# Kernel optimization log

Hardware: AMD Instinct MI355X
Metric: run time of the kernel (lower is better)

## Reference

```python
import jax, jax.numpy as jnp
import numpy as np

B, N, M, V = 256, 16, 128, 64
H, K = 256, 8
TYPES, SPANS = 12, 15          # types 9..20, spans 2..16
TAU = 1.0
NEG = -1e30


def setup_inputs() -> dict:
    key = jax.random.key(0)
    ks = jax.random.split(key, 8)
    decodings = jax.random.normal(ks[0], (B, N, M, V), jnp.float32)
    variables = jax.random.normal(ks[1], (B, N, 30, 3, V), jnp.float32)
    target_types = 9 + jax.random.randint(ks[2], (B,), 0, TYPES)      # [9, 20]
    spans = 2 + jax.random.randint(ks[3], (B,), 0, SPANS)             # [2, 16]
    type_emb_table = jax.random.normal(ks[4], (21, H), jnp.float32)
    W_sem = jax.random.normal(ks[5], (SPANS, TYPES, H, K * (N + 1)), jnp.float32) * 0.05
    b_sem = jnp.zeros((SPANS, TYPES, K * (N + 1)), jnp.float32)
    u = jax.random.uniform(ks[6], (B, K, N + 1), jnp.float32, 1e-9, 1.0)
    gumbel = -jnp.log(-jnp.log(u))
    return dict(decodings=decodings, variables=variables, target_types=target_types,
                spans=spans, type_emb_table=type_emb_table, W_sem=W_sem,
                b_sem=b_sem, gumbel=gumbel)


def _dt_sample(type_emb_table, W_sem, b_sem, gumbel, target_types, spans):
    te = type_emb_table[target_types]                                  # [B,H]
    Wg = W_sem[spans - 2, target_types - 9]                            # [B,H,K*(N+1)]
    bg = b_sem[spans - 2, target_types - 9]                            # [B,K*(N+1)]
    logits = (jnp.einsum('bh,bho->bo', te, Wg) + bg).reshape(B, K, N + 1)
    valid = jnp.arange(N + 1)[None, None, :] < (spans[:, None, None] + 1)
    logits = jnp.where(valid, logits, NEG)
    logp = jax.nn.log_softmax(logits, axis=-1)
    y_soft = jax.nn.softmax((logp + gumbel) / TAU, axis=-1)
    hard = jax.nn.one_hot(jnp.argmax(y_soft, axis=-1), N + 1, dtype=y_soft.dtype)
    dt = hard + y_soft - jax.lax.stop_gradient(y_soft)                 # straight-through
    dt = jnp.where(valid, dt, 0.0)                                     # zeros beyond span+1
    # type 20 uses the fixed start template: template 0 picks decoding 0, rest pick pad
    start = jax.nn.one_hot(jnp.where(jnp.arange(K) == 0, 1, 0), N + 1, dtype=dt.dtype)
    return jnp.where((target_types == 20)[:, None, None], start[None], dt)


def _apply_decoder_template(dt, decodings):
    pad = jnp.zeros((M, V), decodings.dtype).at[:, 0].set(1.0)         # pad token one-hot
    choices = jnp.concatenate(
        [jnp.broadcast_to(pad.reshape(1, 1, M * V), (B, 1, M * V)),
         decodings.reshape(B, N, M * V)], axis=1)                      # [B,N+1,M*V]
    outputs = jnp.einsum('bkn,bnf->bkf', dt, choices).reshape(B, K, M, V)

    jpos = jnp.arange(M, dtype=jnp.int32)

    def step(carry, out_t):                                            # out_t: [B,M,V]
        result, idx = carry
        out_idx = jnp.argmax(out_t, axis=-1)                           # [B,M]
        olen = jnp.max(jnp.where(out_idx != 0, jpos + 1, 0), axis=-1)  # last non-pad + 1
        olen = jnp.minimum(olen, M - idx)
        rel = jpos[None, :] - idx[:, None]                             # [B,M]
        take = (rel >= 0) & (rel < olen[:, None])
        gathered = jnp.take_along_axis(out_t, jnp.clip(rel, 0, M - 1)[:, :, None], axis=1)
        result = jnp.where(take[:, :, None], gathered, result)
        return (result, idx + olen), None

    init = (jnp.zeros((B, M, V), decodings.dtype), jnp.zeros((B,), jnp.int32))
    (result, _), _ = jax.lax.scan(step, init, jnp.moveaxis(outputs, 1, 0))
    return result


def reference(decodings, variables, target_types, spans, type_emb_table, W_sem, b_sem, gumbel):
    dt = _dt_sample(type_emb_table, W_sem, b_sem, gumbel, target_types, spans)
    new_d = _apply_decoder_template(dt, decodings)
    new_v = jnp.zeros((B, 40, 3, V), decodings.dtype)
    return new_d, new_v
```

## Files before the change

kernel.cpp:

```cpp
#include <hip/hip_runtime.h>
#include <cfloat>

constexpr int B_ = 256, N_ = 16, M_ = 128, V_ = 64, H_ = 256, K_ = 8, NP1 = 17;
constexpr int KO = K_ * NP1;
constexpr int TYPES_ = 12;

__global__ __launch_bounds__(256) void fused_template_kernel(
    const float* __restrict__ decodings,
    const int*   __restrict__ target_types,
    const int*   __restrict__ spans,
    const float* __restrict__ type_emb,
    const float* __restrict__ W_sem,
    const float* __restrict__ b_sem,
    const float* __restrict__ gumbel,
    float* __restrict__ out_d,
    float* __restrict__ out_v)
{
    const int b = blockIdx.x;
    const int t = threadIdx.x;

    __shared__ float te[H_];
    __shared__ float score[KO];
    __shared__ int   sel[K_];
    __shared__ int   wave_hi[2];

    const int tt = target_types[b];
    const int sp = spans[b];

    if (tt == 20) {
        if (t < K_) sel[t] = (t == 0) ? 1 : 0;
    } else {
        te[t] = type_emb[tt * H_ + t];
        __syncthreads();
        const int row = (sp - 2) * TYPES_ + (tt - 9);
        if (t < KO) {
            const float* W = W_sem + (size_t)row * H_ * KO + t;
            float acc = b_sem[row * KO + t];
            #pragma unroll 8
            for (int h = 0; h < H_; ++h)
                acc = fmaf(te[h], W[(size_t)h * KO], acc);
            const int n = t % NP1;
            const float g = gumbel[b * KO + t];
            score[t] = (n <= sp) ? (acc + g) : -FLT_MAX;
        }
        __syncthreads();
        if (t < K_) {
            float bv = score[t * NP1];
            int bi = 0;
            for (int n = 1; n < NP1; ++n) {
                float v = score[t * NP1 + n];
                if (v > bv) { bv = v; bi = n; }
            }
            sel[t] = bi;
        }
    }
    __syncthreads();

    int idx = 0;
    for (int k = 0; k < K_; ++k) {
        if (idx >= M_) break;
        const int s = sel[k];
        if (s == 0) continue;
        const float* seq = decodings + ((size_t)b * N_ + (s - 1)) * (M_ * V_);

        int nonpad = 0;
        if (t < M_) {
            const float4* p = reinterpret_cast<const float4*>(seq + t * V_);
            float bv = -FLT_MAX; int bi = 0;
            #pragma unroll
            for (int q = 0; q < V_ / 4; ++q) {
                float4 x = p[q];
                if (x.x > bv) { bv = x.x; bi = 4 * q + 0; }
                if (x.y > bv) { bv = x.y; bi = 4 * q + 1; }
                if (x.z > bv) { bv = x.z; bi = 4 * q + 2; }
                if (x.w > bv) { bv = x.w; bi = 4 * q + 3; }
            }
            nonpad = (bi != 0);
        }
        const unsigned long long mask = __ballot(nonpad);
        if ((t & 63) == 0 && (t >> 6) < 2)
            wave_hi[t >> 6] = mask ? (63 - __clzll(mask)) : -1;
        __syncthreads();
        int olen = (wave_hi[1] >= 0) ? (wave_hi[1] + 65) : (wave_hi[0] + 1);
        olen = min(olen, M_ - idx);

        const int cnt4 = olen * (V_ / 4);
        const float4* src4 = reinterpret_cast<const float4*>(seq);
        float4* dst4 = reinterpret_cast<float4*>(out_d + ((size_t)b * M_ + idx) * V_);
        for (int i = t; i < cnt4; i += 256) dst4[i] = src4[i];
        idx += olen;
        __syncthreads();
    }

    const float4 z = make_float4(0.f, 0.f, 0.f, 0.f);
    float4* db = reinterpret_cast<float4*>(out_d + (size_t)b * M_ * V_);
    for (int i = idx * (V_ / 4) + t; i < M_ * (V_ / 4); i += 256) db[i] = z;
    float4* dv = reinterpret_cast<float4*>(out_v + (size_t)b * (40 * 3 * V_));
    for (int i = t; i < (40 * 3 * V_) / 4; i += 256) dv[i] = z;
}

extern "C" void kernel_launch(void* const* d_in, const int* in_sizes, int n_in,
                              void* d_out, int out_size, void* d_ws, size_t ws_size,
                              hipStream_t stream) {
    const float* decodings    = (const float*)d_in[0];
    const int*   target_types = (const int*)d_in[2];
    const int*   spans        = (const int*)d_in[3];
    const float* type_emb     = (const float*)d_in[4];
    const float* W_sem        = (const float*)d_in[5];
    const float* b_sem        = (const float*)d_in[6];
    const float* gumbel       = (const float*)d_in[7];

    float* out_d = (float*)d_out;
    float* out_v = out_d + (size_t)B_ * M_ * V_;

    fused_template_kernel<<<dim3(B_), dim3(256), 0, stream>>>(
        decodings, target_types, spans, type_emb, W_sem, b_sem, gumbel, out_d, out_v);
}
```

Before: 247.2 us.

## Stage W_sem rows through LDS with all threads and split zeroing into extra blocks

After: 251.0 us. About the same (+1.5%).

```diff
diff --git a/kernel.cpp b/kernel.cpp
--- a/kernel.cpp
+++ b/kernel.cpp
@@ -4,6 +4,8 @@
 constexpr int B_ = 256, N_ = 16, M_ = 128, V_ = 64, H_ = 256, K_ = 8, NP1 = 17;
 constexpr int KO = K_ * NP1;
 constexpr int TYPES_ = 12;
+constexpr int CHUNK = 64;
+constexpr int NV_F4 = (40 * 3 * V_) / 4;
 
 __global__ __launch_bounds__(256) void fused_template_kernel(
     const float* __restrict__ decodings,
@@ -16,9 +18,20 @@
     float* __restrict__ out_d,
     float* __restrict__ out_v)
 {
+    const int t = threadIdx.x;
+    const float4 z = make_float4(0.f, 0.f, 0.f, 0.f);
+
+    if (blockIdx.x >= B_) {
+        const int zb = blockIdx.x - B_;
+        float4* dv = reinterpret_cast<float4*>(out_v + (size_t)zb * (NV_F4 * 4));
+        #pragma unroll
+        for (int i = t; i < NV_F4; i += 256) dv[i] = z;
+        return;
+    }
+
     const int b = blockIdx.x;
-    const int t = threadIdx.x;
 
+    __shared__ float wbuf[CHUNK * KO];
     __shared__ float te[H_];
     __shared__ float score[KO];
     __shared__ int   sel[K_];
@@ -31,14 +44,24 @@
         if (t < K_) sel[t] = (t == 0) ? 1 : 0;
     } else {
         te[t] = type_emb[tt * H_ + t];
-        __syncthreads();
         const int row = (sp - 2) * TYPES_ + (tt - 9);
+        float acc = (t < KO) ? b_sem[row * KO + t] : 0.f;
+
+        for (int c = 0; c < H_; c += CHUNK) {
+            __syncthreads();
+            const float4* src = reinterpret_cast<const float4*>(
+                W_sem + ((size_t)row * H_ + c) * KO);
+            float4* dst = reinterpret_cast<float4*>(wbuf);
+            #pragma unroll
+            for (int i = t; i < CHUNK * KO / 4; i += 256) dst[i] = src[i];
+            __syncthreads();
+            if (t < KO) {
+                #pragma unroll 16
+                for (int h = 0; h < CHUNK; ++h)
+                    acc = fmaf(te[c + h], wbuf[h * KO + t], acc);
+            }
+        }
         if (t < KO) {
-            const float* W = W_sem + (size_t)row * H_ * KO + t;
-            float acc = b_sem[row * KO + t];
-            #pragma unroll 8
-            for (int h = 0; h < H_; ++h)
-                acc = fmaf(te[h], W[(size_t)h * KO], acc);
             const int n = t % NP1;
             const float g = gumbel[b * KO + t];
             score[t] = (n <= sp) ? (acc + g) : -FLT_MAX;
@@ -92,11 +115,8 @@
         __syncthreads();
     }
 
-    const float4 z = make_float4(0.f, 0.f, 0.f, 0.f);
     float4* db = reinterpret_cast<float4*>(out_d + (size_t)b * M_ * V_);
     for (int i = idx * (V_ / 4) + t; i < M_ * (V_ / 4); i += 256) db[i] = z;
-    float4* dv = reinterpret_cast<float4*>(out_v + (size_t)b * (40 * 3 * V_));
-    for (int i = t; i < (40 * 3 * V_) / 4; i += 256) dv[i] = z;
 }
 
 extern "C" void kernel_launch(void* const* d_in, const int* in_sizes, int n_in,
@@ -113,6 +133,6 @@
     float* out_d = (float*)d_out;
     float* out_v = out_d + (size_t)B_ * M_ * V_;
 
-    fused_template_kernel<<<dim3(B_), dim3(256), 0, stream>>>(
+    fused_template_kernel<<<dim3(2 * B_), dim3(256), 0, stream>>>(
         decodings, target_types, spans, type_emb, W_sem, b_sem, gumbel, out_d, out_v);
 }
```
